# Kernel tuning notes

Hardware: AMD Instinct MI355X
Metric: run time of the kernel (lower is better)

The kernel has to match this reference:

```python
import jax, jax.numpy as jnp
import numpy as np

TOKENS, D_MODEL, D_FF, RANK = 16384, 1024, 2816, 16


def setup_inputs() -> dict:
    key = jax.random.key(0)
    ks = jax.random.split(key, 7)
    s = lambda k, shp, scale: jax.random.normal(k, shp, dtype=jnp.float32) * scale
    return {
        "x": s(ks[0], (TOKENS, D_MODEL), 1.0),
        "W_gate_up": s(ks[1], (D_MODEL, 2 * D_FF), 0.02),
        "A_gate_up": s(ks[2], (D_MODEL, RANK), 0.02),
        "B_gate_up": s(ks[3], (RANK, 2 * D_FF), 0.02),
        "W_down": s(ks[4], (D_FF, D_MODEL), 0.02),
        "A_down": s(ks[5], (D_FF, RANK), 0.02),
        "B_down": s(ks[6], (RANK, D_MODEL), 0.02),
    }


def reference(x, W_gate_up, A_gate_up, B_gate_up, W_down, A_down, B_down):
    # gate_up_proj: base GEMM + LoRA low-rank correction
    gate_up = x @ W_gate_up + (x @ A_gate_up) @ B_gate_up  # [T, 2*D_FF]
    gate, up = jnp.split(gate_up, 2, axis=-1)
    h = jax.nn.silu(gate) * up  # SiluAndMul, [T, D_FF]
    # down_proj: base GEMM + LoRA correction
    out = h @ W_down + (h @ A_down) @ B_down  # [T, D_MODEL]
    return out
```

## Files before the change

kernel.cpp:

```cpp
#include <hip/hip_runtime.h>


typedef __bf16 bf16_t;
typedef __bf16 bf16x4 __attribute__((ext_vector_type(4)));
typedef __bf16 bf16x8 __attribute__((ext_vector_type(8)));
typedef float f32x4 __attribute__((ext_vector_type(4)));

#define TOKENS 16384
#define DMODEL 1024
#define DFF    2816
#define N2F    5632

#define BARM() asm volatile("s_barrier" ::: "memory")
#define VMW(n) asm volatile("s_waitcnt vmcnt(" #n ")" ::: "memory")
#define MFMA(d, va, vb) d = __builtin_amdgcn_mfma_f32_16x16x32_bf16(va, vb, d, 0, 0, 0)
#define LD8(p) (*(const bf16x8*)(p))

__device__ __forceinline__ void gload16(const bf16_t* g, bf16_t* l) {
    __builtin_amdgcn_global_load_lds(
        (const __attribute__((address_space(1))) void*)g,
        (__attribute__((address_space(3))) void*)l, 16, 0, 0);
}

template<int KTOT, int NTOT>
__global__ __launch_bounds__(256) void prep_weff(
        const float* __restrict__ W, const float* __restrict__ A,
        const float* __restrict__ B, bf16_t* __restrict__ Wt) {
    __shared__ float Ws[64][65];
    __shared__ float As[64][17];
    __shared__ float Bs[16][64];
    const int t = threadIdx.x;
    const int k0 = blockIdx.x * 64, n0 = blockIdx.y * 64;
    #pragma unroll
    for (int i = 0; i < 16; ++i) {
        int row = i * 4 + t / 64, col = t % 64;
        Ws[row][col] = W[(size_t)(k0 + row) * NTOT + n0 + col];
    }
    #pragma unroll
    for (int i = 0; i < 4; ++i) {
        int idx = i * 256 + t;
        As[idx / 16][idx % 16] = A[(size_t)(k0 + idx / 16) * 16 + idx % 16];
    }
    #pragma unroll
    for (int i = 0; i < 4; ++i) {
        int idx = i * 256 + t;
        Bs[idx / 64][idx % 64] = B[(size_t)(idx / 64) * NTOT + n0 + idx % 64];
    }
    __syncthreads();
    const int kl = t % 64;
    #pragma unroll
    for (int j = 0; j < 16; ++j) {
        int nl = j * 4 + t / 64;
        float val = Ws[kl][nl];
        #pragma unroll
        for (int r = 0; r < 16; ++r) val += As[kl][r] * Bs[r][nl];
        Wt[(size_t)(n0 + nl) * KTOT + k0 + kl] = (bf16_t)val;
    }
}

__global__ __launch_bounds__(256) void conv_bf16(
        const float* __restrict__ in, bf16_t* __restrict__ out, int n4) {
    int i = blockIdx.x * 256 + threadIdx.x;
    if (i < n4) {
        float4 v = ((const float4*)in)[i];
        bf16x4 o;
        o.x = (bf16_t)v.x; o.y = (bf16_t)v.y; o.z = (bf16_t)v.z; o.w = (bf16_t)v.w;
        ((bf16x4*)out)[i] = o;
    }
}

__global__ __launch_bounds__(512, 2) void gemm1(
        const bf16_t* __restrict__ X, const bf16_t* __restrict__ Wt,
        bf16_t* __restrict__ H) {
    __shared__ bf16_t lds[65536];
    const int t = threadIdx.x, l = t & 63;
    const int wid = t >> 6, wr = wid >> 2, wc = wid & 3;
    const int l15 = l & 15, lhi = l >> 4;
    const int wgl = ((int)blockIdx.x & 7) * 176 + ((int)blockIdx.x >> 3);
    const int tf = wgl % 22, tm = wgl / 22;
    const int mbase = tm * 256, fbase = tf * 128;
    const int srow = t >> 2;
    const int sc8 = ((t & 3) ^ (srow & 3)) * 8;
    const bf16_t* gA  = X + (size_t)(mbase + srow) * DMODEL + sc8;
    const bf16_t* gA2 = gA + (size_t)128 * DMODEL;
    const bf16_t* gBg = Wt + (size_t)(fbase + srow) * DMODEL + sc8;
    const bf16_t* gBu = Wt + (size_t)(DFF + fbase + srow) * DMODEL + sc8;
    const int rsw = (lhi ^ (l15 & 3)) * 8;
    const int aoff = (wr * 128 + l15) * 32 + rsw;
    const int boff = 8192 + (wc * 32 + l15) * 32 + rsw;

    f32x4 accg[8][2] = {}, accu[8][2] = {};
    bf16x8 a0[8], g0[2], u0[2], a1[8], g1[2], u1[2];
    const int NT1 = DMODEL / 32;

#define G1_STAGE(kt) do { const int kc = (kt) * 32;                               \
    bf16_t* p = lds + (((kt) & 3) << 14) + wid * 512;                             \
    gload16(gA  + kc, p);                                                         \
    gload16(gA2 + kc, p + 4096);                                                  \
    gload16(gBg + kc, p + 8192);                                                  \
    gload16(gBu + kc, p + 12288); } while (0)
#define G1_READ(aa, gg, uu, bi) do {                                              \
    const bf16_t* _pa = lds + ((bi) << 14) + aoff;                                \
    aa[0] = LD8(_pa);        aa[1] = LD8(_pa + 512);                              \
    aa[2] = LD8(_pa + 1024); aa[3] = LD8(_pa + 1536);                             \
    aa[4] = LD8(_pa + 2048); aa[5] = LD8(_pa + 2560);                             \
    aa[6] = LD8(_pa + 3072); aa[7] = LD8(_pa + 3584);                             \
    const bf16_t* _pb = lds + ((bi) << 14) + boff;                                \
    gg[0] = LD8(_pb);        gg[1] = LD8(_pb + 512);                              \
    uu[0] = LD8(_pb + 4096); uu[1] = LD8(_pb + 4608); } while (0)
#define G1_MFMA(aa, gg, uu) do { __builtin_amdgcn_s_setprio(1);                   \
    _Pragma("unroll")                                                             \
    for (int m = 0; m < 8; ++m) {                                                 \
        MFMA(accg[m][0], aa[m], gg[0]); MFMA(accu[m][0], aa[m], uu[0]);           \
        MFMA(accg[m][1], aa[m], gg[1]); MFMA(accu[m][1], aa[m], uu[1]);           \
    }                                                                             \
    __builtin_amdgcn_s_setprio(0); } while (0)
#define G1_ITER(kt, aaU, ggU, uuU, aaR, ggR, uuR) do {                            \
    VMW(4); BARM();                                                               \
    if ((kt) + 3 < NT1) G1_STAGE((kt) + 3);                                       \
    G1_READ(aaR, ggR, uuR, ((kt) + 1) & 3);                                       \
    G1_MFMA(aaU, ggU, uuU); } while (0)

    G1_STAGE(0); G1_STAGE(1); G1_STAGE(2);
    VMW(8); BARM();
    G1_READ(a0, g0, u0, 0);
    for (int kt2 = 0; kt2 < NT1 - 2; kt2 += 2) {
        G1_ITER(kt2,     a0, g0, u0, a1, g1, u1);
        G1_ITER(kt2 + 1, a1, g1, u1, a0, g0, u0);
    }
    VMW(0); BARM();
    G1_READ(a1, g1, u1, (NT1 - 1) & 3);
    G1_MFMA(a0, g0, u0);
    G1_MFMA(a1, g1, u1);
#undef G1_STAGE
#undef G1_READ
#undef G1_MFMA
#undef G1_ITER

    #pragma unroll
    for (int m = 0; m < 8; ++m)
        #pragma unroll
        for (int n = 0; n < 2; ++n)
            #pragma unroll
            for (int r = 0; r < 4; ++r) {
                int row = mbase + wr * 128 + m * 16 + lhi * 4 + r;
                int col = fbase + wc * 32 + n * 16 + l15;
                float g = accg[m][n][r], u = accu[m][n][r];
                H[(size_t)row * DFF + col] = (bf16_t)(g / (1.0f + __expf(-g)) * u);
            }
}

__global__ __launch_bounds__(512, 2) void gemm2(
        const bf16_t* __restrict__ Hm, const bf16_t* __restrict__ Wt,
        float* __restrict__ O) {
    __shared__ bf16_t lds[65536];
    const int t = threadIdx.x, l = t & 63;
    const int wid = t >> 6, wr = wid >> 2, wc = wid & 3;
    const int l15 = l & 15, lhi = l >> 4;
    const int wgl = ((int)blockIdx.x & 7) * 32 + ((int)blockIdx.x >> 3);
    const int tn = wgl % 4, tm = wgl / 4;
    const int mbase = tm * 256, nbase = tn * 256;
    const int srow = t >> 2;
    const int sc8 = ((t & 3) ^ (srow & 3)) * 8;
    const bf16_t* gA  = Hm + (size_t)(mbase + srow) * DFF + sc8;
    const bf16_t* gA2 = gA + (size_t)128 * DFF;
    const bf16_t* gB  = Wt + (size_t)(nbase + srow) * DFF + sc8;
    const bf16_t* gB2 = gB + (size_t)128 * DFF;
    const int rsw = (lhi ^ (l15 & 3)) * 8;
    const int aoff = (wr * 128 + l15) * 32 + rsw;
    const int boff = 8192 + (wc * 64 + l15) * 32 + rsw;

    f32x4 acc[8][4] = {};
    bf16x8 a0[8], b0[4], a1[8], b1[4];
    const int NT2 = DFF / 32;

#define G2_STAGE(kt) do { const int kc = (kt) * 32;                               \
    bf16_t* p = lds + (((kt) & 3) << 14) + wid * 512;                             \
    gload16(gA  + kc, p);                                                         \
    gload16(gA2 + kc, p + 4096);                                                  \
    gload16(gB  + kc, p + 8192);                                                  \
    gload16(gB2 + kc, p + 12288); } while (0)
#define G2_READ(aa, bb, bi) do {                                                  \
    const bf16_t* _pa = lds + ((bi) << 14) + aoff;                                \
    aa[0] = LD8(_pa);        aa[1] = LD8(_pa + 512);                              \
    aa[2] = LD8(_pa + 1024); aa[3] = LD8(_pa + 1536);                             \
    aa[4] = LD8(_pa + 2048); aa[5] = LD8(_pa + 2560);                             \
    aa[6] = LD8(_pa + 3072); aa[7] = LD8(_pa + 3584);                             \
    const bf16_t* _pb = lds + ((bi) << 14) + boff;                                \
    bb[0] = LD8(_pb);        bb[1] = LD8(_pb + 512);                              \
    bb[2] = LD8(_pb + 1024); bb[3] = LD8(_pb + 1536); } while (0)
#define G2_MFMA(aa, bb) do { __builtin_amdgcn_s_setprio(1);                       \
    _Pragma("unroll")                                                             \
    for (int m = 0; m < 8; ++m) {                                                 \
        MFMA(acc[m][0], aa[m], bb[0]); MFMA(acc[m][1], aa[m], bb[1]);             \
        MFMA(acc[m][2], aa[m], bb[2]); MFMA(acc[m][3], aa[m], bb[3]);             \
    }                                                                             \
    __builtin_amdgcn_s_setprio(0); } while (0)
#define G2_ITER(kt, aaU, bbU, aaR, bbR) do {                                      \
    VMW(4); BARM();                                                               \
    if ((kt) + 3 < NT2) G2_STAGE((kt) + 3);                                       \
    G2_READ(aaR, bbR, ((kt) + 1) & 3);                                            \
    G2_MFMA(aaU, bbU); } while (0)

    G2_STAGE(0); G2_STAGE(1); G2_STAGE(2);
    VMW(8); BARM();
    G2_READ(a0, b0, 0);
    for (int kt2 = 0; kt2 < NT2 - 2; kt2 += 2) {
        G2_ITER(kt2,     a0, b0, a1, b1);
        G2_ITER(kt2 + 1, a1, b1, a0, b0);
    }
    VMW(0); BARM();
    G2_READ(a1, b1, (NT2 - 1) & 3);
    G2_MFMA(a0, b0);
    G2_MFMA(a1, b1);
#undef G2_STAGE
#undef G2_READ
#undef G2_MFMA
#undef G2_ITER

    #pragma unroll
    for (int m = 0; m < 8; ++m)
        #pragma unroll
        for (int n = 0; n < 4; ++n)
            #pragma unroll
            for (int r = 0; r < 4; ++r) {
                int row = mbase + wr * 128 + m * 16 + lhi * 4 + r;
                int col = nbase + wc * 64 + n * 16 + l15;
                O[(size_t)row * DMODEL + col] = acc[m][n][r];
            }
}

extern "C" void kernel_launch(void* const* d_in, const int* in_sizes, int n_in,
                              void* d_out, int out_size, void* d_ws, size_t ws_size,
                              hipStream_t stream) {
    const float* x   = (const float*)d_in[0];
    const float* Wgu = (const float*)d_in[1];
    const float* Agu = (const float*)d_in[2];
    const float* Bgu = (const float*)d_in[3];
    const float* Wd  = (const float*)d_in[4];
    const float* Ad  = (const float*)d_in[5];
    const float* Bd  = (const float*)d_in[6];
    float* out = (float*)d_out;
    char* ws = (char*)d_ws;

    bf16_t* wgut = (bf16_t*)(ws);
    bf16_t* wdt  = (bf16_t*)(ws + 11534336);
    bf16_t* xb   = (bf16_t*)(ws + 17301504);
    bf16_t* hb   = (bf16_t*)(ws + 50855936);

    prep_weff<DMODEL, N2F><<<dim3(DMODEL / 64, N2F / 64), 256, 0, stream>>>(
        Wgu, Agu, Bgu, wgut);
    prep_weff<DFF, DMODEL><<<dim3(DFF / 64, DMODEL / 64), 256, 0, stream>>>(
        Wd, Ad, Bd, wdt);
    conv_bf16<<<(TOKENS * DMODEL / 4) / 256, 256, 0, stream>>>(
        x, xb, TOKENS * DMODEL / 4);
    gemm1<<<22 * 64, 512, 0, stream>>>(xb, wgut, hb);
    gemm2<<<8 * 32, 512, 0, stream>>>(hb, wdt, out);
}
```

Measured before the change: 350.3 us.

## Restructure GEMMs to 4-wave blocks with BK=64 double-buffered LDS and sched barriers

Both GEMM kernels move from 8 waves with a 4-stage BK=32 ring to 4 waves per block, each computing a larger per-wave tile (128x128 of output), with a double-buffered BK=64 LDS pipeline using an 8-way XOR swizzle. Explicit sched_group_barrier patterns interleave LDS reads, global-to-LDS loads and MFMAs. The aim is more MFMA work per LDS read and fewer barriers per unit of K. In exchange, per-thread register use roughly doubles, occupancy drops to one block per CU, and a full vmcnt(0) wait every iteration may expose global-load latency.

```diff
diff --git a/kernel.cpp b/kernel.cpp
--- a/kernel.cpp
+++ b/kernel.cpp
@@ -12,9 +12,17 @@
 #define N2F    5632
 
 #define BARM() asm volatile("s_barrier" ::: "memory")
-#define VMW(n) asm volatile("s_waitcnt vmcnt(" #n ")" ::: "memory")
+#define VMW0() asm volatile("s_waitcnt vmcnt(0)" ::: "memory")
 #define MFMA(d, va, vb) d = __builtin_amdgcn_mfma_f32_16x16x32_bf16(va, vb, d, 0, 0, 0)
 #define LD8(p) (*(const bf16x8*)(p))
+#define SGB(m, n) __builtin_amdgcn_sched_group_barrier(m, n, 0)
+#define SGB_PAT() do {                                                            \
+    SGB(0x010, 16); SGB(0x100, 16);                                               \
+    SGB(0x008, 8); SGB(0x100, 2); SGB(0x008, 8); SGB(0x100, 2);                   \
+    SGB(0x008, 8); SGB(0x100, 2); SGB(0x008, 8); SGB(0x100, 2);                   \
+    SGB(0x008, 8); SGB(0x100, 2); SGB(0x008, 8); SGB(0x100, 2);                   \
+    SGB(0x008, 8); SGB(0x100, 2); SGB(0x008, 8); SGB(0x100, 2);                   \
+    SGB(0x008, 64); } while (0)
 
 __device__ __forceinline__ void gload16(const bf16_t* g, bf16_t* l) {
     __builtin_amdgcn_global_load_lds(
@@ -69,163 +77,159 @@
     }
 }
 
-__global__ __launch_bounds__(512, 2) void gemm1(
+__global__ __launch_bounds__(256, 1) void gemm1(
         const bf16_t* __restrict__ X, const bf16_t* __restrict__ Wt,
         bf16_t* __restrict__ H) {
     __shared__ bf16_t lds[65536];
     const int t = threadIdx.x, l = t & 63;
-    const int wid = t >> 6, wr = wid >> 2, wc = wid & 3;
+    const int wid = t >> 6, wr = wid >> 1, wc = wid & 1;
     const int l15 = l & 15, lhi = l >> 4;
     const int wgl = ((int)blockIdx.x & 7) * 176 + ((int)blockIdx.x >> 3);
     const int tf = wgl % 22, tm = wgl / 22;
     const int mbase = tm * 256, fbase = tf * 128;
-    const int srow = t >> 2;
-    const int sc8 = ((t & 3) ^ (srow & 3)) * 8;
-    const bf16_t* gA  = X + (size_t)(mbase + srow) * DMODEL + sc8;
-    const bf16_t* gA2 = gA + (size_t)128 * DMODEL;
-    const bf16_t* gBg = Wt + (size_t)(fbase + srow) * DMODEL + sc8;
-    const bf16_t* gBu = Wt + (size_t)(DFF + fbase + srow) * DMODEL + sc8;
-    const int rsw = (lhi ^ (l15 & 3)) * 8;
-    const int aoff = (wr * 128 + l15) * 32 + rsw;
-    const int boff = 8192 + (wc * 32 + l15) * 32 + rsw;
-
-    f32x4 accg[8][2] = {}, accu[8][2] = {};
-    bf16x8 a0[8], g0[2], u0[2], a1[8], g1[2], u1[2];
-    const int NT1 = DMODEL / 32;
-
-#define G1_STAGE(kt) do { const int kc = (kt) * 32;                               \
-    bf16_t* p = lds + (((kt) & 3) << 14) + wid * 512;                             \
-    gload16(gA  + kc, p);                                                         \
-    gload16(gA2 + kc, p + 4096);                                                  \
-    gload16(gBg + kc, p + 8192);                                                  \
-    gload16(gBu + kc, p + 12288); } while (0)
-#define G1_READ(aa, gg, uu, bi) do {                                              \
-    const bf16_t* _pa = lds + ((bi) << 14) + aoff;                                \
-    aa[0] = LD8(_pa);        aa[1] = LD8(_pa + 512);                              \
-    aa[2] = LD8(_pa + 1024); aa[3] = LD8(_pa + 1536);                             \
-    aa[4] = LD8(_pa + 2048); aa[5] = LD8(_pa + 2560);                             \
-    aa[6] = LD8(_pa + 3072); aa[7] = LD8(_pa + 3584);                             \
-    const bf16_t* _pb = lds + ((bi) << 14) + boff;                                \
-    gg[0] = LD8(_pb);        gg[1] = LD8(_pb + 512);                              \
-    uu[0] = LD8(_pb + 4096); uu[1] = LD8(_pb + 4608); } while (0)
-#define G1_MFMA(aa, gg, uu) do { __builtin_amdgcn_s_setprio(1);                   \
-    _Pragma("unroll")                                                             \
-    for (int m = 0; m < 8; ++m) {                                                 \
-        MFMA(accg[m][0], aa[m], gg[0]); MFMA(accu[m][0], aa[m], uu[0]);           \
-        MFMA(accg[m][1], aa[m], gg[1]); MFMA(accu[m][1], aa[m], uu[1]);           \
-    }                                                                             \
-    __builtin_amdgcn_s_setprio(0); } while (0)
-#define G1_ITER(kt, aaU, ggU, uuU, aaR, ggR, uuR) do {                            \
-    VMW(4); BARM();                                                               \
-    if ((kt) + 3 < NT1) G1_STAGE((kt) + 3);                                       \
-    G1_READ(aaR, ggR, uuR, ((kt) + 1) & 3);                                       \
-    G1_MFMA(aaU, ggU, uuU); } while (0)
-
-    G1_STAGE(0); G1_STAGE(1); G1_STAGE(2);
-    VMW(8); BARM();
-    G1_READ(a0, g0, u0, 0);
-    for (int kt2 = 0; kt2 < NT1 - 2; kt2 += 2) {
-        G1_ITER(kt2,     a0, g0, u0, a1, g1, u1);
-        G1_ITER(kt2 + 1, a1, g1, u1, a0, g0, u0);
-    }
-    VMW(0); BARM();
-    G1_READ(a1, g1, u1, (NT1 - 1) & 3);
-    G1_MFMA(a0, g0, u0);
-    G1_MFMA(a1, g1, u1);
+    const int sr = t >> 3;
+    const int scol = ((t & 7) ^ (sr & 7)) * 8;
+    const int swz0 = ((lhi ^ (l15 & 7))) * 8;
+    const int aro = (wr * 128 + l15) * 64 + swz0;
+    const int bro = (wc * 64 + l15) * 64 + swz0;
+
+    f32x4 accg[8][4] = {}, accu[8][4] = {};
+    bf16x8 a[8], bg[4], bu[4];
+    bf16_t* bufR = lds;
+    bf16_t* bufS = lds + 32768;
+    const int NT1 = DMODEL / 64;
+
+#define G1_STAGE(kt, buf) do { const int kc = (kt) * 64 + scol;                   \
+    _Pragma("unroll")                                                             \
+    for (int i = 0; i < 8; ++i)                                                   \
+        gload16(X + (size_t)(mbase + i * 32 + sr) * DMODEL + kc,                  \
+                (buf) + i * 2048 + t * 8);                                        \
+    _Pragma("unroll")                                                             \
+    for (int i = 0; i < 4; ++i)                                                   \
+        gload16(Wt + (size_t)(fbase + i * 32 + sr) * DMODEL + kc,                 \
+                (buf) + 16384 + i * 2048 + t * 8);                                \
+    _Pragma("unroll")                                                             \
+    for (int i = 0; i < 4; ++i)                                                   \
+        gload16(Wt + (size_t)(DFF + fbase + i * 32 + sr) * DMODEL + kc,           \
+                (buf) + 24576 + i * 2048 + t * 8); } while (0)
+#define G1_READK(kh, buf) do { const int _x = (kh) * 32;                          \
+    const bf16_t* _A = (buf);                                                     \
+    a[0] = LD8(_A + (aro ^ _x));          a[1] = LD8(_A + (aro ^ _x) + 1024);     \
+    a[2] = LD8(_A + (aro ^ _x) + 2048);   a[3] = LD8(_A + (aro ^ _x) + 3072);     \
+    a[4] = LD8(_A + (aro ^ _x) + 4096);   a[5] = LD8(_A + (aro ^ _x) + 5120);     \
+    a[6] = LD8(_A + (aro ^ _x) + 6144);   a[7] = LD8(_A + (aro ^ _x) + 7168);     \
+    const bf16_t* _B = (buf) + 16384;                                             \
+    bg[0] = LD8(_B + (bro ^ _x));         bg[1] = LD8(_B + (bro ^ _x) + 1024);    \
+    bg[2] = LD8(_B + (bro ^ _x) + 2048);  bg[3] = LD8(_B + (bro ^ _x) + 3072);    \
+    bu[0] = LD8(_B + (bro ^ _x) + 8192);  bu[1] = LD8(_B + (bro ^ _x) + 9216);    \
+    bu[2] = LD8(_B + (bro ^ _x) + 10240); bu[3] = LD8(_B + (bro ^ _x) + 11264); } while (0)
+#define G1_MFMAK() do {                                                           \
+    _Pragma("unroll")                                                             \
+    for (int m = 0; m < 8; ++m)                                                   \
+        _Pragma("unroll")                                                         \
+        for (int f = 0; f < 4; ++f) {                                             \
+            MFMA(accg[m][f], a[m], bg[f]);                                        \
+            MFMA(accu[m][f], a[m], bu[f]);                                        \
+        } } while (0)
+
+    G1_STAGE(0, bufR);
+    VMW0(); BARM();
+    for (int kt = 0; kt < NT1; ++kt) {
+        if (kt + 1 < NT1) G1_STAGE(kt + 1, bufS);
+        G1_READK(0, bufR); G1_MFMAK();
+        G1_READK(1, bufR); G1_MFMAK();
+        SGB_PAT();
+        VMW0(); BARM();
+        bf16_t* _tp = bufR; bufR = bufS; bufS = _tp;
+    }
 #undef G1_STAGE
-#undef G1_READ
-#undef G1_MFMA
-#undef G1_ITER
+#undef G1_READK
+#undef G1_MFMAK
 
     #pragma unroll
     for (int m = 0; m < 8; ++m)
         #pragma unroll
-        for (int n = 0; n < 2; ++n)
+        for (int f = 0; f < 4; ++f)
             #pragma unroll
             for (int r = 0; r < 4; ++r) {
                 int row = mbase + wr * 128 + m * 16 + lhi * 4 + r;
-                int col = fbase + wc * 32 + n * 16 + l15;
-                float g = accg[m][n][r], u = accu[m][n][r];
+                int col = fbase + wc * 64 + f * 16 + l15;
+                float g = accg[m][f][r], u = accu[m][f][r];
                 H[(size_t)row * DFF + col] = (bf16_t)(g / (1.0f + __expf(-g)) * u);
             }
 }
 
-__global__ __launch_bounds__(512, 2) void gemm2(
+__global__ __launch_bounds__(256, 1) void gemm2(
         const bf16_t* __restrict__ Hm, const bf16_t* __restrict__ Wt,
         float* __restrict__ O) {
     __shared__ bf16_t lds[65536];
     const int t = threadIdx.x, l = t & 63;
-    const int wid = t >> 6, wr = wid >> 2, wc = wid & 3;
+    const int wid = t >> 6, wr = wid >> 1, wc = wid & 1;
     const int l15 = l & 15, lhi = l >> 4;
     const int wgl = ((int)blockIdx.x & 7) * 32 + ((int)blockIdx.x >> 3);
     const int tn = wgl % 4, tm = wgl / 4;
     const int mbase = tm * 256, nbase = tn * 256;
-    const int srow = t >> 2;
-    const int sc8 = ((t & 3) ^ (srow & 3)) * 8;
-    const bf16_t* gA  = Hm + (size_t)(mbase + srow) * DFF + sc8;
-    const bf16_t* gA2 = gA + (size_t)128 * DFF;
-    const bf16_t* gB  = Wt + (size_t)(nbase + srow) * DFF + sc8;
-    const bf16_t* gB2 = gB + (size_t)128 * DFF;
-    const int rsw = (lhi ^ (l15 & 3)) * 8;
-    const int aoff = (wr * 128 + l15) * 32 + rsw;
-    const int boff = 8192 + (wc * 64 + l15) * 32 + rsw;
-
-    f32x4 acc[8][4] = {};
-    bf16x8 a0[8], b0[4], a1[8], b1[4];
-    const int NT2 = DFF / 32;
-
-#define G2_STAGE(kt) do { const int kc = (kt) * 32;                               \
-    bf16_t* p = lds + (((kt) & 3) << 14) + wid * 512;                             \
-    gload16(gA  + kc, p);                                                         \
-    gload16(gA2 + kc, p + 4096);                                                  \
-    gload16(gB  + kc, p + 8192);                                                  \
-    gload16(gB2 + kc, p + 12288); } while (0)
-#define G2_READ(aa, bb, bi) do {                                                  \
-    const bf16_t* _pa = lds + ((bi) << 14) + aoff;                                \
-    aa[0] = LD8(_pa);        aa[1] = LD8(_pa + 512);                              \
-    aa[2] = LD8(_pa + 1024); aa[3] = LD8(_pa + 1536);                             \
-    aa[4] = LD8(_pa + 2048); aa[5] = LD8(_pa + 2560);                             \
-    aa[6] = LD8(_pa + 3072); aa[7] = LD8(_pa + 3584);                             \
-    const bf16_t* _pb = lds + ((bi) << 14) + boff;                                \
-    bb[0] = LD8(_pb);        bb[1] = LD8(_pb + 512);                              \
-    bb[2] = LD8(_pb + 1024); bb[3] = LD8(_pb + 1536); } while (0)
-#define G2_MFMA(aa, bb) do { __builtin_amdgcn_s_setprio(1);                       \
-    _Pragma("unroll")                                                             \
-    for (int m = 0; m < 8; ++m) {                                                 \
-        MFMA(acc[m][0], aa[m], bb[0]); MFMA(acc[m][1], aa[m], bb[1]);             \
-        MFMA(acc[m][2], aa[m], bb[2]); MFMA(acc[m][3], aa[m], bb[3]);             \
-    }                                                                             \
-    __builtin_amdgcn_s_setprio(0); } while (0)
-#define G2_ITER(kt, aaU, bbU, aaR, bbR) do {                                      \
-    VMW(4); BARM();                                                               \
-    if ((kt) + 3 < NT2) G2_STAGE((kt) + 3);                                       \
-    G2_READ(aaR, bbR, ((kt) + 1) & 3);                                            \
-    G2_MFMA(aaU, bbU); } while (0)
-
-    G2_STAGE(0); G2_STAGE(1); G2_STAGE(2);
-    VMW(8); BARM();
-    G2_READ(a0, b0, 0);
-    for (int kt2 = 0; kt2 < NT2 - 2; kt2 += 2) {
-        G2_ITER(kt2,     a0, b0, a1, b1);
-        G2_ITER(kt2 + 1, a1, b1, a0, b0);
-    }
-    VMW(0); BARM();
-    G2_READ(a1, b1, (NT2 - 1) & 3);
-    G2_MFMA(a0, b0);
-    G2_MFMA(a1, b1);
+    const int sr = t >> 3;
+    const int scol = ((t & 7) ^ (sr & 7)) * 8;
+    const int swz0 = ((lhi ^ (l15 & 7))) * 8;
+    const int aro = (wr * 128 + l15) * 64 + swz0;
+    const int bro = (wc * 128 + l15) * 64 + swz0;
+
+    f32x4 acc[8][8] = {};
+    bf16x8 a[8], b[8];
+    bf16_t* bufR = lds;
+    bf16_t* bufS = lds + 32768;
+    const int NT2 = DFF / 64;
+
+#define G2_STAGE(kt, buf) do { const int kc = (kt) * 64 + scol;                   \
+    _Pragma("unroll")                                                             \
+    for (int i = 0; i < 8; ++i)                                                   \
+        gload16(Hm + (size_t)(mbase + i * 32 + sr) * DFF + kc,                    \
+                (buf) + i * 2048 + t * 8);                                        \
+    _Pragma("unroll")                                                             \
+    for (int i = 0; i < 8; ++i)                                                   \
+        gload16(Wt + (size_t)(nbase + i * 32 + sr) * DFF + kc,                    \
+                (buf) + 16384 + i * 2048 + t * 8); } while (0)
+#define G2_READK(kh, buf) do { const int _x = (kh) * 32;                          \
+    const bf16_t* _A = (buf);                                                     \
+    a[0] = LD8(_A + (aro ^ _x));          a[1] = LD8(_A + (aro ^ _x) + 1024);     \
+    a[2] = LD8(_A + (aro ^ _x) + 2048);   a[3] = LD8(_A + (aro ^ _x) + 3072);     \
+    a[4] = LD8(_A + (aro ^ _x) + 4096);   a[5] = LD8(_A + (aro ^ _x) + 5120);     \
+    a[6] = LD8(_A + (aro ^ _x) + 6144);   a[7] = LD8(_A + (aro ^ _x) + 7168);     \
+    const bf16_t* _B = (buf) + 16384;                                             \
+    b[0] = LD8(_B + (bro ^ _x));          b[1] = LD8(_B + (bro ^ _x) + 1024);     \
+    b[2] = LD8(_B + (bro ^ _x) + 2048);   b[3] = LD8(_B + (bro ^ _x) + 3072);     \
+    b[4] = LD8(_B + (bro ^ _x) + 4096);   b[5] = LD8(_B + (bro ^ _x) + 5120);     \
+    b[6] = LD8(_B + (bro ^ _x) + 6144);   b[7] = LD8(_B + (bro ^ _x) + 7168); } while (0)
+#define G2_MFMAK() do {                                                           \
+    _Pragma("unroll")                                                             \
+    for (int m = 0; m < 8; ++m)                                                   \
+        _Pragma("unroll")                                                         \
+        for (int n = 0; n < 8; ++n)                                               \
+            MFMA(acc[m][n], a[m], b[n]); } while (0)
+
+    G2_STAGE(0, bufR);
+    VMW0(); BARM();
+    for (int kt = 0; kt < NT2; ++kt) {
+        if (kt + 1 < NT2) G2_STAGE(kt + 1, bufS);
+        G2_READK(0, bufR); G2_MFMAK();
+        G2_READK(1, bufR); G2_MFMAK();
+        SGB_PAT();
+        VMW0(); BARM();
+        bf16_t* _tp = bufR; bufR = bufS; bufS = _tp;
+    }
 #undef G2_STAGE
-#undef G2_READ
-#undef G2_MFMA
-#undef G2_ITER
+#undef G2_READK
+#undef G2_MFMAK
 
     #pragma unroll
     for (int m = 0; m < 8; ++m)
         #pragma unroll
-        for (int n = 0; n < 4; ++n)
+        for (int n = 0; n < 8; ++n)
             #pragma unroll
             for (int r = 0; r < 4; ++r) {
                 int row = mbase + wr * 128 + m * 16 + lhi * 4 + r;
-                int col = nbase + wc * 64 + n * 16 + l15;
+                int col = nbase + wc * 128 + n * 16 + l15;
                 O[(size_t)row * DMODEL + col] = acc[m][n][r];
             }
 }
@@ -254,6 +258,6 @@
         Wd, Ad, Bd, wdt);
     conv_bf16<<<(TOKENS * DMODEL / 4) / 256, 256, 0, stream>>>(
         x, xb, TOKENS * DMODEL / 4);
-    gemm1<<<22 * 64, 512, 0, stream>>>(xb, wgut, hb);
-    gemm2<<<8 * 32, 512, 0, stream>>>(hb, wdt, out);
-}
+    gemm1<<<22 * 64, 256, 0, stream>>>(xb, wgut, hb);
+    gemm2<<<4 * 64, 256, 0, stream>>>(hb, wdt, out);
+}
```

New measurement: 361.8 us. 1.03x slower.
